# Performance work log

Measured on AMD Instinct MI355X. Metric: run time of the kernel, lower is better.

The kernel has to match this reference:

```python
import jax, jax.numpy as jnp
import numpy as np

N_NODES = 100000
N_EDGES = 1600000
N_GRAPHS = 512
F_IN, HID, EMB = 256, 64, 2


def gcn_layer(h, src, dst, W, b, n_nodes):
    # PyG GCNConv: h' = D^{-1/2} (A + I) D^{-1/2} (h W) + b
    h = h @ W  # [N, out]
    loop = jnp.arange(n_nodes)
    s = jnp.concatenate([src, loop])
    d = jnp.concatenate([dst, loop])
    deg = jax.ops.segment_sum(jnp.ones_like(d, dtype=h.dtype), d, num_segments=n_nodes)
    dinv = jnp.where(deg > 0, jax.lax.rsqrt(deg), 0.0)
    norm = dinv[s] * dinv[d]  # [E+N]
    msg = h[s] * norm[:, None]  # gather + scale
    return jax.ops.segment_sum(msg, d, num_segments=n_nodes) + b


def setup_inputs() -> dict:
    key = jax.random.key(0)
    k1, k2, k3, k4, k5, k6 = jax.random.split(key, 6)
    x = jax.random.normal(k1, (N_NODES, F_IN), dtype=jnp.float32)
    edge_index = jax.random.randint(k2, (2, N_EDGES), 0, N_NODES, dtype=jnp.int64)
    batch = jnp.sort(jax.random.randint(k3, (N_NODES,), 0, N_GRAPHS, dtype=jnp.int64))
    # Glorot-ish init for layer weights
    W1 = jax.random.normal(k4, (F_IN, HID), dtype=jnp.float32) / np.sqrt(F_IN)
    b1 = jnp.zeros((HID,), dtype=jnp.float32)
    W2 = jax.random.normal(k5, (HID, EMB), dtype=jnp.float32) / np.sqrt(HID)
    b2 = jnp.zeros((EMB,), dtype=jnp.float32)
    return {"x": x, "edge_index": edge_index, "batch": batch,
            "W1": W1, "b1": b1, "W2": W2, "b2": b2}


def reference(x, edge_index, batch, W1, b1, W2, b2):
    n = x.shape[0]
    src, dst = edge_index[0], edge_index[1]
    h = gcn_layer(x, src, dst, W1, b1, n)
    h = jax.nn.relu(h)
    h = gcn_layer(h, src, dst, W2, b2, n)
    # global_mean_pool over graph ids
    sums = jax.ops.segment_sum(h, batch, num_segments=N_GRAPHS)
    cnts = jax.ops.segment_sum(jnp.ones((n,), dtype=h.dtype), batch, num_segments=N_GRAPHS)
    return sums / jnp.maximum(cnts, 1.0)[:, None]
```

## Files before the change

### kernel.cpp

```cpp
#include <hip/hip_runtime.h>
#include <hip/hip_bf16.h>

#define FIN 256
#define HID 64
#define EMB 2
#define BKB 9
#define BKSZ 512
#define MAXBK 256
#define NBLK 256

typedef __bf16 bf16x8 __attribute__((ext_vector_type(8)));
typedef float  f32x16 __attribute__((ext_vector_type(16)));
typedef unsigned short u16x8 __attribute__((ext_vector_type(8)));

static __device__ __forceinline__ unsigned short f2bf(float f) {
    union { float f; unsigned int u; } v; v.f = f;
    unsigned int u = v.u;
    unsigned int r = (u + 0x7fffu + ((u >> 16) & 1u)) >> 16;
    return (unsigned short)r;
}
static __device__ __forceinline__ float bf2f(unsigned short h) {
    union { unsigned int u; float f; } v; v.u = ((unsigned int)h) << 16;
    return v.f;
}

__global__ __launch_bounds__(256) void bin_hist_kernel(
        const int* __restrict__ dst, int* __restrict__ counts, int E, int chunk, int NBK) {
    __shared__ int hist[MAXBK];
    int tid = threadIdx.x;
    for (int b = tid; b < NBK; b += 256) hist[b] = 0;
    __syncthreads();
    int e0 = blockIdx.x * chunk, e1 = min(e0 + chunk, E);
    if (e0 < e1) {
        const int4* d4 = (const int4*)(dst + e0);
        int nv = (e1 - e0) >> 2;
        for (int i = tid; i < nv; i += 256) {
            int4 v = d4[i];
            atomicAdd(&hist[v.x >> BKB], 1);
            atomicAdd(&hist[v.y >> BKB], 1);
            atomicAdd(&hist[v.z >> BKB], 1);
            atomicAdd(&hist[v.w >> BKB], 1);
        }
        for (int i = e0 + (nv << 2) + tid; i < e1; i += 256)
            atomicAdd(&hist[dst[i] >> BKB], 1);
    }
    __syncthreads();
    for (int b = tid; b < NBK; b += 256) counts[b * gridDim.x + blockIdx.x] = hist[b];
}

__global__ __launch_bounds__(256) void scan_local_kernel(
        int* __restrict__ counts, int* __restrict__ btot) {
    __shared__ int s[256];
    const int b = blockIdx.x, tid = threadIdx.x;
    int v = counts[b * NBLK + tid];
    s[tid] = v;
    __syncthreads();
    for (int off = 1; off < 256; off <<= 1) {
        int t = (tid >= off) ? s[tid - off] : 0;
        __syncthreads();
        s[tid] += t;
        __syncthreads();
    }
    counts[b * NBLK + tid] = s[tid] - v;
    if (tid == 255) btot[b] = s[255];
}

__global__ __launch_bounds__(256) void scan_tot_kernel(
        const int* __restrict__ btot, int* __restrict__ bucketBase,
        float* __restrict__ sums, int NBK, int nzero) {
    __shared__ int s[256];
    const int tid = threadIdx.x;
    int v = (tid < NBK) ? btot[tid] : 0;
    s[tid] = v;
    __syncthreads();
    for (int off = 1; off < 256; off <<= 1) {
        int t = (tid >= off) ? s[tid - off] : 0;
        __syncthreads();
        s[tid] += t;
        __syncthreads();
    }
    if (tid < NBK) bucketBase[tid] = s[tid] - v;
    if (tid == NBK - 1) bucketBase[NBK] = s[tid];
    for (int i = tid; i < nzero; i += 256) sums[i] = 0.f;
}

__global__ __launch_bounds__(256) void bin_scatter_kernel(
        const int* __restrict__ src, const int* __restrict__ dst,
        const int* __restrict__ counts, const int* __restrict__ bucketBase,
        unsigned* __restrict__ ebuf, int E, int chunk, int NBK) {
    __shared__ int cur[MAXBK];
    int tid = threadIdx.x;
    for (int b = tid; b < NBK; b += 256)
        cur[b] = bucketBase[b] + counts[b * gridDim.x + blockIdx.x];
    __syncthreads();
    int e0 = blockIdx.x * chunk, e1 = min(e0 + chunk, E);
    if (e0 >= e1) return;
    const int4* s4 = (const int4*)(src + e0);
    const int4* d4 = (const int4*)(dst + e0);
    int nv = (e1 - e0) >> 2;
    for (int i = tid; i < nv; i += 256) {
        int4 sv = s4[i], dv = d4[i];
        int b0 = dv.x >> BKB;
        int p0 = atomicAdd(&cur[b0], 1);
        ebuf[p0] = ((unsigned)sv.x << BKB) | (unsigned)(dv.x & (BKSZ - 1));
        int b1 = dv.y >> BKB;
        int p1 = atomicAdd(&cur[b1], 1);
        ebuf[p1] = ((unsigned)sv.y << BKB) | (unsigned)(dv.y & (BKSZ - 1));
        int b2 = dv.z >> BKB;
        int p2 = atomicAdd(&cur[b2], 1);
        ebuf[p2] = ((unsigned)sv.z << BKB) | (unsigned)(dv.z & (BKSZ - 1));
        int b3 = dv.w >> BKB;
        int p3 = atomicAdd(&cur[b3], 1);
        ebuf[p3] = ((unsigned)sv.w << BKB) | (unsigned)(dv.w & (BKSZ - 1));
    }
    for (int i = e0 + (nv << 2) + tid; i < e1; i += 256) {
        int s = src[i], d = dst[i];
        int b = d >> BKB;
        int pos = atomicAdd(&cur[b], 1);
        ebuf[pos] = ((unsigned)s << BKB) | (unsigned)(d & (BKSZ - 1));
    }
}

__global__ __launch_bounds__(256) void build_kernel(
        const unsigned* __restrict__ ebuf, const int* __restrict__ bucketBase,
        int* __restrict__ rowptr, float* __restrict__ dinv, int* __restrict__ csr,
        int N, int E) {
    __shared__ int hist[BKSZ];
    __shared__ int scanb[256];
    __shared__ int cur[BKSZ];
    const int b = blockIdx.x, tid = threadIdx.x;
    const int r0 = bucketBase[b];
    const int r1 = bucketBase[b + 1];
    const int nb0 = b * BKSZ;

    hist[tid] = 0; hist[tid + 256] = 0;
    __syncthreads();
    for (int i = r0 + tid; i < r1; i += 256)
        atomicAdd(&hist[ebuf[i] & (BKSZ - 1u)], 1);
    __syncthreads();

    int h0 = hist[2 * tid], h1 = hist[2 * tid + 1];
    if (nb0 + 2 * tid < N)     dinv[nb0 + 2 * tid]     = rsqrtf((float)h0 + 1.f);
    if (nb0 + 2 * tid + 1 < N) dinv[nb0 + 2 * tid + 1] = rsqrtf((float)h1 + 1.f);
    scanb[tid] = h0 + h1;
    __syncthreads();
    for (int off = 1; off < 256; off <<= 1) {
        int t = (tid >= off) ? scanb[tid - off] : 0;
        __syncthreads();
        scanb[tid] += t;
        __syncthreads();
    }
    int base0 = scanb[tid] - (h0 + h1);
    int o0 = base0, o1 = base0 + h0;
    cur[2 * tid] = o0; cur[2 * tid + 1] = o1;
    if (nb0 + 2 * tid < N)     rowptr[nb0 + 2 * tid]     = r0 + o0;
    if (nb0 + 2 * tid + 1 < N) rowptr[nb0 + 2 * tid + 1] = r0 + o1;
    if (nb0 + BKSZ >= N && tid == 0) rowptr[N] = E;
    __syncthreads();
    for (int i = r0 + tid; i < r1; i += 256) {
        unsigned u = ebuf[i];
        int loc = (int)(u & (BKSZ - 1u));
        int p = atomicAdd(&cur[loc], 1);
        csr[r0 + p] = (int)(u >> BKB);
    }
}

__global__ __launch_bounds__(256) void gemm1_kernel(
        const float* __restrict__ x, const float* __restrict__ W,
        const float* __restrict__ dinv, unsigned short* __restrict__ h1b, int N) {
    __shared__ __align__(16) __bf16 A_hi[2 * 4 * 64 * 8];
    __shared__ __align__(16) __bf16 A_lo[2 * 4 * 64 * 8];
    __shared__ __align__(16) __bf16 B_hi[2 * 4 * 64 * 8];
    __shared__ __align__(16) __bf16 B_lo[2 * 4 * 64 * 8];

    const int tid = threadIdx.x;
    const int base = blockIdx.x * 64;
    const int w = tid >> 6;
    const int l = tid & 63;
    const int mg = w >> 1, ng = w & 1;

    f32x16 acc = {};

    const int r  = tid & 63;
    const int ks = tid >> 6;
    const int rl = r & 31, rh = r >> 5;

    for (int ch = 0; ch < 4; ++ch) {
        const int ck0 = ch * 64;
        __syncthreads();
        {
            int row = base + r;
            float f[16];
            if (row < N) {
                const float* xp = &x[(size_t)row * FIN + ck0 + ks * 16];
                float4 v0 = *(const float4*)(xp + 0);
                float4 v1 = *(const float4*)(xp + 4);
                float4 v2 = *(const float4*)(xp + 8);
                float4 v3 = *(const float4*)(xp + 12);
                f[0]=v0.x; f[1]=v0.y; f[2]=v0.z; f[3]=v0.w;
                f[4]=v1.x; f[5]=v1.y; f[6]=v1.z; f[7]=v1.w;
                f[8]=v2.x; f[9]=v2.y; f[10]=v2.z; f[11]=v2.w;
                f[12]=v3.x; f[13]=v3.y; f[14]=v3.z; f[15]=v3.w;
            } else {
                #pragma unroll
                for (int q = 0; q < 16; ++q) f[q] = 0.f;
            }
            bf16x8 ha, hb, la, lb;
            #pragma unroll
            for (int q = 0; q < 8; ++q) {
                __bf16 h0 = (__bf16)f[q];
                ha[q] = h0; la[q] = (__bf16)(f[q] - (float)h0);
                __bf16 h1v = (__bf16)f[q + 8];
                hb[q] = h1v; lb[q] = (__bf16)(f[q + 8] - (float)h1v);
            }
            int ra = ((rh * 4 + ks) * 64 + rl) * 8;
            int rb = ((rh * 4 + ks) * 64 + 32 + rl) * 8;
            *(bf16x8*)&A_hi[ra] = ha; *(bf16x8*)&A_hi[rb] = hb;
            *(bf16x8*)&A_lo[ra] = la; *(bf16x8*)&A_lo[rb] = lb;
        }
        {
            const float* wp = &W[(size_t)(ck0 + ks * 16) * HID + r];
            float f[16];
            #pragma unroll
            for (int q = 0; q < 16; ++q) f[q] = wp[q * HID];
            bf16x8 ha, hb, la, lb;
            #pragma unroll
            for (int q = 0; q < 8; ++q) {
                __bf16 h0 = (__bf16)f[q];
                ha[q] = h0; la[q] = (__bf16)(f[q] - (float)h0);
                __bf16 h1v = (__bf16)f[q + 8];
                hb[q] = h1v; lb[q] = (__bf16)(f[q + 8] - (float)h1v);
            }
            int ra = ((rh * 4 + ks) * 64 + rl) * 8;
            int rb = ((rh * 4 + ks) * 64 + 32 + rl) * 8;
            *(bf16x8*)&B_hi[ra] = ha; *(bf16x8*)&B_hi[rb] = hb;
            *(bf16x8*)&B_lo[ra] = la; *(bf16x8*)&B_lo[rb] = lb;
        }
        __syncthreads();

        #pragma unroll
        for (int s = 0; s < 4; ++s) {
            bf16x8 a_h = *(const bf16x8*)&A_hi[((mg * 4 + s) * 64 + l) * 8];
            bf16x8 a_l = *(const bf16x8*)&A_lo[((mg * 4 + s) * 64 + l) * 8];
            bf16x8 b_h = *(const bf16x8*)&B_hi[((ng * 4 + s) * 64 + l) * 8];
            bf16x8 b_l = *(const bf16x8*)&B_lo[((ng * 4 + s) * 64 + l) * 8];
            acc = __builtin_amdgcn_mfma_f32_32x32x16_bf16(a_h, b_h, acc, 0, 0, 0);
            acc = __builtin_amdgcn_mfma_f32_32x32x16_bf16(a_h, b_l, acc, 0, 0, 0);
            acc = __builtin_amdgcn_mfma_f32_32x32x16_bf16(a_l, b_h, acc, 0, 0, 0);
        }
    }

    const int col = l & 31;
    const int rbase = 4 * (l >> 5);
    #pragma unroll
    for (int reg = 0; reg < 16; ++reg) {
        int row = (reg & 3) + 8 * (reg >> 2) + rbase;
        int node = base + mg * 32 + row;
        if (node < N)
            h1b[(size_t)node * HID + ng * 32 + col] = f2bf(acc[reg] * dinv[node]);
    }
}

__global__ __launch_bounds__(256) void agg1_layer2_kernel(
        const int* __restrict__ rowptr, const int* __restrict__ csr,
        const unsigned short* __restrict__ h1b,
        const float* __restrict__ dinv, const float* __restrict__ b1,
        const float* __restrict__ W2, float* __restrict__ h2, int N) {
    long t = (long)blockIdx.x * blockDim.x + threadIdx.x;
    int n = (int)(t >> 3);
    int li = threadIdx.x & 7;
    if (n >= N) return;
    const u16x8* h18 = (const u16x8*)h1b;

    float di = dinv[n];
    u16x8 sl = h18[(size_t)n * 8 + li];
    float v[8];
    #pragma unroll
    for (int k = 0; k < 8; ++k) v[k] = bf2f(sl[k]);

    int j0 = rowptr[n], j1 = rowptr[n + 1];
    int j = j0;
    for (; j + 3 < j1; j += 4) {
        int s0 = csr[j], s1 = csr[j + 1], s2 = csr[j + 2], s3 = csr[j + 3];
        u16x8 g0 = h18[(size_t)s0 * 8 + li];
        u16x8 g1 = h18[(size_t)s1 * 8 + li];
        u16x8 g2 = h18[(size_t)s2 * 8 + li];
        u16x8 g3 = h18[(size_t)s3 * 8 + li];
        #pragma unroll
        for (int k = 0; k < 8; ++k)
            v[k] += bf2f(g0[k]) + bf2f(g1[k]) + bf2f(g2[k]) + bf2f(g3[k]);
    }
    for (; j < j1; ++j) {
        u16x8 g = h18[(size_t)csr[j] * 8 + li];
        #pragma unroll
        for (int k = 0; k < 8; ++k) v[k] += bf2f(g[k]);
    }

    const float4 ba = *(const float4*)&b1[li * 8];
    const float4 bb = *(const float4*)&b1[li * 8 + 4];
    v[0] = fmaxf(di * v[0] + ba.x, 0.f); v[1] = fmaxf(di * v[1] + ba.y, 0.f);
    v[2] = fmaxf(di * v[2] + ba.z, 0.f); v[3] = fmaxf(di * v[3] + ba.w, 0.f);
    v[4] = fmaxf(di * v[4] + bb.x, 0.f); v[5] = fmaxf(di * v[5] + bb.y, 0.f);
    v[6] = fmaxf(di * v[6] + bb.z, 0.f); v[7] = fmaxf(di * v[7] + bb.w, 0.f);

    const float4* W24 = (const float4*)W2;
    float r0 = 0.f, r1 = 0.f;
    #pragma unroll
    for (int k = 0; k < 4; ++k) {
        float4 wq = W24[li * 4 + k];
        r0 += v[2 * k] * wq.x + v[2 * k + 1] * wq.z;
        r1 += v[2 * k] * wq.y + v[2 * k + 1] * wq.w;
    }
    #pragma unroll
    for (int off = 1; off < 8; off <<= 1) {
        r0 += __shfl_xor(r0, off);
        r1 += __shfl_xor(r1, off);
    }
    if (li == 0) *(float2*)&h2[(size_t)n * EMB] = make_float2(r0 * di, r1 * di);
}

__global__ __launch_bounds__(256) void agg2_pool_kernel(
        const int* __restrict__ rowptr, const int* __restrict__ csr,
        const float* __restrict__ h2,
        const float* __restrict__ dinv, const float* __restrict__ b2,
        const int* __restrict__ batch,
        float* __restrict__ sums, float* __restrict__ cntf, int N) {
    int n = blockIdx.x * blockDim.x + threadIdx.x;
    int lane = threadIdx.x & 63;
    const float2* h2v = (const float2*)h2;
    float v0 = 0.f, v1 = 0.f, c = 0.f;
    int g = -1;
    if (n < N) {
        float di = dinv[n];
        float2 hs = h2v[n];
        v0 = hs.x; v1 = hs.y;
        int j0 = rowptr[n], j1 = rowptr[n + 1];
        int j = j0;
        for (; j + 3 < j1; j += 4) {
            int s0 = csr[j], s1 = csr[j + 1], s2 = csr[j + 2], s3 = csr[j + 3];
            float2 a = h2v[s0], b = h2v[s1], cc = h2v[s2], d = h2v[s3];
            v0 += a.x + b.x + cc.x + d.x;
            v1 += a.y + b.y + cc.y + d.y;
        }
        for (; j < j1; ++j) {
            float2 hv = h2v[csr[j]];
            v0 += hv.x; v1 += hv.y;
        }
        v0 = di * v0 + b2[0];
        v1 = di * v1 + b2[1];
        g = batch[n];
        c = 1.f;
    }
    #pragma unroll
    for (int off = 1; off < 64; off <<= 1) {
        int gg = __shfl_up(g, off);
        float t0 = __shfl_up(v0, off);
        float t1 = __shfl_up(v1, off);
        float tc = __shfl_up(c, off);
        if (lane >= off && gg == g) { v0 += t0; v1 += t1; c += tc; }
    }
    int gn = __shfl_down(g, 1);
    if (g >= 0 && (lane == 63 || gn != g)) {
        atomicAdd(&sums[g * EMB + 0], v0);
        atomicAdd(&sums[g * EMB + 1], v1);
        atomicAdd(&cntf[g], c);
    }
}

__global__ void final_kernel(const float* __restrict__ sums, const float* __restrict__ cntf,
                             float* __restrict__ out, int G) {
    int g = blockIdx.x * blockDim.x + threadIdx.x;
    if (g >= G) return;
    float c = fmaxf(cntf[g], 1.0f);
    out[g * EMB + 0] = sums[g * EMB + 0] / c;
    out[g * EMB + 1] = sums[g * EMB + 1] / c;
}

extern "C" void kernel_launch(void* const* d_in, const int* in_sizes, int n_in,
                              void* d_out, int out_size, void* d_ws, size_t ws_size,
                              hipStream_t stream) {
    const float* x     = (const float*)d_in[0];
    const int*   ei    = (const int*)d_in[1];
    const int*   batch = (const int*)d_in[2];
    const float* W1    = (const float*)d_in[3];
    const float* b1    = (const float*)d_in[4];
    const float* W2    = (const float*)d_in[5];
    const float* b2    = (const float*)d_in[6];
    float* out = (float*)d_out;

    const int N = in_sizes[0] / FIN;
    const int E = in_sizes[1] / 2;
    const int G = out_size / EMB;
    const int* src = ei;
    const int* dst = ei + E;

    const int NBK = (N + BKSZ - 1) / BKSZ;
    const int chunk = (((E + NBLK - 1) / NBLK) + 3) & ~3;

    char* p = (char*)d_ws;
    auto take = [&](size_t bytes) { char* r = p; p += (bytes + 15) & ~(size_t)15; return r; };
    int*      counts = (int*)take(sizeof(int) * NBK * NBLK);
    int*      btot   = (int*)take(sizeof(int) * NBK);
    int*      bucketBase = (int*)take(sizeof(int) * (NBK + 1));
    unsigned* ebuf   = (unsigned*)take(sizeof(unsigned) * E);
    int*      csr    = (int*)take(sizeof(int) * E);
    int*      rowptr = (int*)take(sizeof(int) * (N + 1));
    float*    dinv   = (float*)take(sizeof(float) * N);
    unsigned short* h1b = (unsigned short*)take(sizeof(unsigned short) * (size_t)N * HID);
    float*    h2     = (float*)take(sizeof(float) * (size_t)N * EMB);
    float*    sums   = (float*)take(sizeof(float) * G * EMB);
    float*    cntf   = (float*)take(sizeof(float) * G);

    bin_hist_kernel<<<NBLK, 256, 0, stream>>>(dst, counts, E, chunk, NBK);
    scan_local_kernel<<<NBK, 256, 0, stream>>>(counts, btot);
    scan_tot_kernel<<<1, 256, 0, stream>>>(btot, bucketBase, sums, NBK, 3 * G);
    bin_scatter_kernel<<<NBLK, 256, 0, stream>>>(src, dst, counts, bucketBase, ebuf, E, chunk, NBK);
    build_kernel<<<NBK, 256, 0, stream>>>(ebuf, bucketBase, rowptr, dinv, csr, N, E);
    gemm1_kernel<<<(N + 63) / 64, 256, 0, stream>>>(x, W1, dinv, h1b, N);
    agg1_layer2_kernel<<<(int)(((long)N * 8 + 255) / 256), 256, 0, stream>>>(
        rowptr, csr, h1b, dinv, b1, W2, h2, N);
    agg2_pool_kernel<<<(N + 255) / 256, 256, 0, stream>>>(
        rowptr, csr, h2, dinv, b2, batch, sums, cntf, N);
    final_kernel<<<(G + 255) / 256, 256, 0, stream>>>(sums, cntf, out, G);
}
```

Before: 290.2 us.

## Pre-split W1 into bf16 hi/lo once and deepen gather unrolling

Extra blocks appended to the histogram launch convert W1 once into bf16 hi/lo fragments stored in MFMA-ready order in global memory. The GEMM then reads B fragments directly from global (L2-resident) instead of every block reloading, splitting and staging W through shared memory. This removes per-block W conversion work and halves the shared-memory footprint. Separately, both aggregation kernels gain an 8-way unrolled neighbor gather to put more loads in flight, at the cost of more registers.

```diff
diff --git a/kernel.cpp b/kernel.cpp
--- a/kernel.cpp
+++ b/kernel.cpp
@@ -8,6 +8,7 @@
 #define BKSZ 512
 #define MAXBK 256
 #define NBLK 256
+#define WPREP 8
 
 typedef __bf16 bf16x8 __attribute__((ext_vector_type(8)));
 typedef float  f32x16 __attribute__((ext_vector_type(16)));
@@ -25,7 +26,25 @@
 }
 
 __global__ __launch_bounds__(256) void bin_hist_kernel(
-        const int* __restrict__ dst, int* __restrict__ counts, int E, int chunk, int NBK) {
+        const int* __restrict__ dst, int* __restrict__ counts,
+        const float* __restrict__ W, __bf16* __restrict__ Bh, __bf16* __restrict__ Bl,
+        int E, int chunk, int NBK) {
+    if (blockIdx.x >= NBLK) {
+        int t = (blockIdx.x - NBLK) * 256 + threadIdx.x;
+        int ch = t >> 9, g = (t >> 6) & 7, m = t & 63;
+        int kbase = ch * 64 + (g & 3) * 16 + ((m >> 5) << 3);
+        int n = ((g >> 2) << 5) + (m & 31);
+        bf16x8 hi, lo;
+        #pragma unroll
+        for (int q = 0; q < 8; ++q) {
+            float w = W[(size_t)(kbase + q) * HID + n];
+            __bf16 h = (__bf16)w;
+            hi[q] = h; lo[q] = (__bf16)(w - (float)h);
+        }
+        *(bf16x8*)&Bh[(size_t)t * 8] = hi;
+        *(bf16x8*)&Bl[(size_t)t * 8] = lo;
+        return;
+    }
     __shared__ int hist[MAXBK];
     int tid = threadIdx.x;
     for (int b = tid; b < NBK; b += 256) hist[b] = 0;
@@ -45,7 +64,7 @@
             atomicAdd(&hist[dst[i] >> BKB], 1);
     }
     __syncthreads();
-    for (int b = tid; b < NBK; b += 256) counts[b * gridDim.x + blockIdx.x] = hist[b];
+    for (int b = tid; b < NBK; b += 256) counts[b * NBLK + blockIdx.x] = hist[b];
 }
 
 __global__ __launch_bounds__(256) void scan_local_kernel(
@@ -91,7 +110,7 @@
     __shared__ int cur[MAXBK];
     int tid = threadIdx.x;
     for (int b = tid; b < NBK; b += 256)
-        cur[b] = bucketBase[b] + counts[b * gridDim.x + blockIdx.x];
+        cur[b] = bucketBase[b] + counts[b * NBLK + blockIdx.x];
     __syncthreads();
     int e0 = blockIdx.x * chunk, e1 = min(e0 + chunk, E);
     if (e0 >= e1) return;
@@ -166,18 +185,20 @@
 }
 
 __global__ __launch_bounds__(256) void gemm1_kernel(
-        const float* __restrict__ x, const float* __restrict__ W,
+        const float* __restrict__ x,
+        const __bf16* __restrict__ Bh, const __bf16* __restrict__ Bl,
         const float* __restrict__ dinv, unsigned short* __restrict__ h1b, int N) {
     __shared__ __align__(16) __bf16 A_hi[2 * 4 * 64 * 8];
     __shared__ __align__(16) __bf16 A_lo[2 * 4 * 64 * 8];
-    __shared__ __align__(16) __bf16 B_hi[2 * 4 * 64 * 8];
-    __shared__ __align__(16) __bf16 B_lo[2 * 4 * 64 * 8];
 
     const int tid = threadIdx.x;
     const int base = blockIdx.x * 64;
     const int w = tid >> 6;
     const int l = tid & 63;
     const int mg = w >> 1, ng = w & 1;
+
+    const bf16x8* Bh8 = (const bf16x8*)Bh;
+    const bf16x8* Bl8 = (const bf16x8*)Bl;
 
     f32x16 acc = {};
 
@@ -218,32 +239,15 @@
             *(bf16x8*)&A_hi[ra] = ha; *(bf16x8*)&A_hi[rb] = hb;
             *(bf16x8*)&A_lo[ra] = la; *(bf16x8*)&A_lo[rb] = lb;
         }
-        {
-            const float* wp = &W[(size_t)(ck0 + ks * 16) * HID + r];
-            float f[16];
-            #pragma unroll
-            for (int q = 0; q < 16; ++q) f[q] = wp[q * HID];
-            bf16x8 ha, hb, la, lb;
-            #pragma unroll
-            for (int q = 0; q < 8; ++q) {
-                __bf16 h0 = (__bf16)f[q];
-                ha[q] = h0; la[q] = (__bf16)(f[q] - (float)h0);
-                __bf16 h1v = (__bf16)f[q + 8];
-                hb[q] = h1v; lb[q] = (__bf16)(f[q + 8] - (float)h1v);
-            }
-            int ra = ((rh * 4 + ks) * 64 + rl) * 8;
-            int rb = ((rh * 4 + ks) * 64 + 32 + rl) * 8;
-            *(bf16x8*)&B_hi[ra] = ha; *(bf16x8*)&B_hi[rb] = hb;
-            *(bf16x8*)&B_lo[ra] = la; *(bf16x8*)&B_lo[rb] = lb;
-        }
         __syncthreads();
 
         #pragma unroll
         for (int s = 0; s < 4; ++s) {
             bf16x8 a_h = *(const bf16x8*)&A_hi[((mg * 4 + s) * 64 + l) * 8];
             bf16x8 a_l = *(const bf16x8*)&A_lo[((mg * 4 + s) * 64 + l) * 8];
-            bf16x8 b_h = *(const bf16x8*)&B_hi[((ng * 4 + s) * 64 + l) * 8];
-            bf16x8 b_l = *(const bf16x8*)&B_lo[((ng * 4 + s) * 64 + l) * 8];
+            int bv = (ch * 8 + ng * 4 + s) * 64 + l;
+            bf16x8 b_h = Bh8[bv];
+            bf16x8 b_l = Bl8[bv];
             acc = __builtin_amdgcn_mfma_f32_32x32x16_bf16(a_h, b_h, acc, 0, 0, 0);
             acc = __builtin_amdgcn_mfma_f32_32x32x16_bf16(a_h, b_l, acc, 0, 0, 0);
             acc = __builtin_amdgcn_mfma_f32_32x32x16_bf16(a_l, b_h, acc, 0, 0, 0);
@@ -280,6 +284,23 @@
 
     int j0 = rowptr[n], j1 = rowptr[n + 1];
     int j = j0;
+    for (; j + 7 < j1; j += 8) {
+        int s0 = csr[j],     s1 = csr[j + 1], s2 = csr[j + 2], s3 = csr[j + 3];
+        int s4 = csr[j + 4], s5 = csr[j + 5], s6 = csr[j + 6], s7 = csr[j + 7];
+        u16x8 g0 = h18[(size_t)s0 * 8 + li];
+        u16x8 g1 = h18[(size_t)s1 * 8 + li];
+        u16x8 g2 = h18[(size_t)s2 * 8 + li];
+        u16x8 g3 = h18[(size_t)s3 * 8 + li];
+        u16x8 g4 = h18[(size_t)s4 * 8 + li];
+        u16x8 g5 = h18[(size_t)s5 * 8 + li];
+        u16x8 g6 = h18[(size_t)s6 * 8 + li];
+        u16x8 g7 = h18[(size_t)s7 * 8 + li];
+        #pragma unroll
+        for (int k = 0; k < 8; ++k) {
+            v[k] += bf2f(g0[k]) + bf2f(g1[k]) + bf2f(g2[k]) + bf2f(g3[k]);
+            v[k] += bf2f(g4[k]) + bf2f(g5[k]) + bf2f(g6[k]) + bf2f(g7[k]);
+        }
+    }
     for (; j + 3 < j1; j += 4) {
         int s0 = csr[j], s1 = csr[j + 1], s2 = csr[j + 2], s3 = csr[j + 3];
         u16x8 g0 = h18[(size_t)s0 * 8 + li];
@@ -336,6 +357,16 @@
         v0 = hs.x; v1 = hs.y;
         int j0 = rowptr[n], j1 = rowptr[n + 1];
         int j = j0;
+        for (; j + 7 < j1; j += 8) {
+            int s0 = csr[j],     s1 = csr[j + 1], s2 = csr[j + 2], s3 = csr[j + 3];
+            int s4 = csr[j + 4], s5 = csr[j + 5], s6 = csr[j + 6], s7 = csr[j + 7];
+            float2 a = h2v[s0], b = h2v[s1], cc = h2v[s2], d = h2v[s3];
+            float2 e = h2v[s4], f = h2v[s5], gg2 = h2v[s6], h = h2v[s7];
+            v0 += a.x + b.x + cc.x + d.x;
+            v1 += a.y + b.y + cc.y + d.y;
+            v0 += e.x + f.x + gg2.x + h.x;
+            v1 += e.y + f.y + gg2.y + h.y;
+        }
         for (; j + 3 < j1; j += 4) {
             int s0 = csr[j], s1 = csr[j + 1], s2 = csr[j + 2], s3 = csr[j + 3];
             float2 a = h2v[s0], b = h2v[s1], cc = h2v[s2], d = h2v[s3];
@@ -410,13 +441,15 @@
     float*    h2     = (float*)take(sizeof(float) * (size_t)N * EMB);
     float*    sums   = (float*)take(sizeof(float) * G * EMB);
     float*    cntf   = (float*)take(sizeof(float) * G);
-
-    bin_hist_kernel<<<NBLK, 256, 0, stream>>>(dst, counts, E, chunk, NBK);
+    __bf16*   Bh     = (__bf16*)take(sizeof(__bf16) * 4 * 8 * 64 * 8);
+    __bf16*   Bl     = (__bf16*)take(sizeof(__bf16) * 4 * 8 * 64 * 8);
+
+    bin_hist_kernel<<<NBLK + WPREP, 256, 0, stream>>>(dst, counts, W1, Bh, Bl, E, chunk, NBK);
     scan_local_kernel<<<NBK, 256, 0, stream>>>(counts, btot);
     scan_tot_kernel<<<1, 256, 0, stream>>>(btot, bucketBase, sums, NBK, 3 * G);
     bin_scatter_kernel<<<NBLK, 256, 0, stream>>>(src, dst, counts, bucketBase, ebuf, E, chunk, NBK);
     build_kernel<<<NBK, 256, 0, stream>>>(ebuf, bucketBase, rowptr, dinv, csr, N, E);
-    gemm1_kernel<<<(N + 63) / 64, 256, 0, stream>>>(x, W1, dinv, h1b, N);
+    gemm1_kernel<<<(N + 63) / 64, 256, 0, stream>>>(x, Bh, Bl, dinv, h1b, N);
     agg1_layer2_kernel<<<(int)(((long)N * 8 + 255) / 256), 256, 0, stream>>>(
         rowptr, csr, h1b, dinv, b1, W2, h2, N);
     agg2_pool_kernel<<<(N + 255) / 256, 256, 0, stream>>>(
```

New measurement: 288.8 us (median of 2 runs). About the same (-0.5%).
